# Optimization experiments

Measured on AMD Instinct MI355X. Metric: run time of the kernel, lower is better.

The kernel has to match this reference:

```python
import jax, jax.numpy as jnp
import numpy as np

EPS = 1e-8  # torch.cosine_similarity default eps


def setup_inputs() -> dict:
    key = jax.random.key(0)
    k1, k2 = jax.random.split(key)
    B, S, C, W = 8, 75, 64, 19
    support_x = jax.random.normal(k1, (B, S, C, W, W), dtype=jnp.float32)
    query_x = jax.random.normal(k2, (B, S, C, W, W), dtype=jnp.float32)
    return {"support_x": support_x, "query_x": query_x}


def reference(support_x, query_x):
    # support_x, query_x: [B, S, C, W, W]
    # For each support spatial location (i,j), cosine-similarity of its C-vector
    # against every query spatial location (p,q), then max over (p,q).
    B, S, C, W, _ = support_x.shape
    s_norm = jnp.linalg.norm(support_x, axis=2)  # [B,S,W,W]
    q_norm = jnp.linalg.norm(query_x, axis=2)    # [B,S,W,W]
    # Pairwise dot products over channels: [B,S,Wi,Wj,Wp,Wq]
    num = jnp.einsum('bscij,bscpq->bsijpq', support_x, query_x)
    denom = jnp.maximum(s_norm[:, :, :, :, None, None] * q_norm[:, :, None, None, :, :], EPS)
    sim = num / denom
    out = jnp.max(sim, axis=(-2, -1))  # max over query spatial grid -> [B,S,W,W]
    # loop order was i (rows) then j (cols), concatenated on last dim == row-major reshape
    return out.reshape(B, S, W * W)
```

## Files before the change

### kernel.cpp

```cpp
#include <hip/hip_runtime.h>
#include <hip/hip_bf16.h>
#include <stdint.h>

#define WW   361
#define CCH  64
#define MH   128
#define NP   368
#define NBS  600

typedef __attribute__((ext_vector_type(8))) short short8;
typedef __attribute__((ext_vector_type(4))) float f32x4;


__device__ __forceinline__ float stage_row(const float* __restrict__ gp,
                                           unsigned short* __restrict__ dst, int sw) {
  float a0 = 0.f, a1 = 0.f, a2 = 0.f, a3 = 0.f;
  #pragma unroll
  for (int h = 0; h < 2; ++h) {
    float v[32];
    #pragma unroll
    for (int j = 0; j < 32; ++j) v[j] = gp[(h * 32 + j) * WW];
    #pragma unroll
    for (int j = 0; j < 32; j += 4) {
      a0 += v[j] * v[j];     a1 += v[j+1] * v[j+1];
      a2 += v[j+2] * v[j+2]; a3 += v[j+3] * v[j+3];
    }
    #pragma unroll
    for (int c0 = 0; c0 < 4; ++c0) {
      const int c = h * 4 + c0;
      unsigned int u[4];
      #pragma unroll
      for (int jj = 0; jj < 4; ++jj) {
        __hip_bfloat162 b2 =
            __float22bfloat162_rn(make_float2(v[c0 * 8 + 2 * jj], v[c0 * 8 + 2 * jj + 1]));
        u[jj] = *(unsigned int*)&b2;
      }
      *(uint4*)&dst[(c ^ sw) * 8] = make_uint4(u[0], u[1], u[2], u[3]);
    }
  }
  return rsqrtf(a0 + a1 + a2 + a3);
}

__device__ __forceinline__ void zero_row(unsigned short* __restrict__ dst) {
  #pragma unroll
  for (int c = 0; c < 8; ++c)
    *(uint4*)&dst[c * 8] = make_uint4(0u, 0u, 0u, 0u);
}

__global__ __launch_bounds__(512, 4) void cossim_max_kernel(
    const float* __restrict__ support, const float* __restrict__ query,
    float* __restrict__ out)
{
  __shared__ __align__(16) unsigned short S_sh[MH * CCH];
  __shared__ __align__(16) unsigned short Q_sh[NP * CCH];
  __shared__ float inv_s[MH];
  __shared__ float inv_q[NP];

  const int tid   = threadIdx.x;
  const int bs    = blockIdx.x / 3;
  const int third = blockIdx.x % 3;
  const int mBase = third * MH;

  const float* sg = support + (size_t)bs * (WW * CCH);
  const float* qg = query   + (size_t)bs * (WW * CCH);

  if (tid < NP) {
    const int m = tid;
    if (m < WW) {
      inv_q[m] = stage_row(qg + m, &Q_sh[m * CCH], m & 7);
    } else {
      zero_row(&Q_sh[m * CCH]);
      inv_q[m] = 0.f;
    }
  } else if (tid < NP + MH) {
    const int mL = tid - NP;
    const int mG = mBase + mL;
    if (mG < WW) {
      inv_s[mL] = stage_row(sg + mG, &S_sh[mL * CCH], mL & 7);
    } else {
      zero_row(&S_sh[mL * CCH]);
      inv_s[mL] = 0.f;
    }
  }
  __syncthreads();

  const int lane = tid & 63;
  const int wv   = tid >> 6;
  const int l15  = lane & 15;
  const int quad = lane >> 4;

  short8 af[2];
  {
    const int m = 16 * wv + l15;
    #pragma unroll
    for (int s = 0; s < 2; ++s) {
      const int c = 4 * s + quad;
      af[s] = *(const short8*)&S_sh[m * CCH + ((c ^ (m & 7)) * 8)];
    }
  }

  f32x4 mx = {-3e38f, -3e38f, -3e38f, -3e38f};

  for (int pt = 0; pt < NP / 16; ++pt) {
    const int n  = 16 * pt + l15;
    const int sw = l15 & 7;
    short8 b0 = *(const short8*)&Q_sh[n * CCH + (((0 + quad) ^ sw) * 8)];
    short8 b1 = *(const short8*)&Q_sh[n * CCH + (((4 + quad) ^ sw) * 8)];
    f32x4 acc = {0.f, 0.f, 0.f, 0.f};
    acc = __builtin_amdgcn_mfma_f32_16x16x32_bf16(af[0], b0, acc, 0, 0, 0);
    acc = __builtin_amdgcn_mfma_f32_16x16x32_bf16(af[1], b1, acc, 0, 0, 0);
    const float qs   = inv_q[n];
    const float bias = (n < WW) ? 0.f : -1e30f;
    #pragma unroll
    for (int r = 0; r < 4; ++r) mx[r] = fmaxf(mx[r], acc[r] * qs + bias);
  }

  #pragma unroll
  for (int d = 1; d < 16; d <<= 1) {
    #pragma unroll
    for (int r = 0; r < 4; ++r) mx[r] = fmaxf(mx[r], __shfl_xor(mx[r], d));
  }

  if (l15 == 0) {
    #pragma unroll
    for (int r = 0; r < 4; ++r) {
      const int mL = 16 * wv + 4 * quad + r;
      const int iG = mBase + mL;
      if (iG < WW) out[(size_t)bs * WW + iG] = mx[r] * inv_s[mL];
    }
  }
}

extern "C" void kernel_launch(void* const* d_in, const int* in_sizes, int n_in,
                              void* d_out, int out_size, void* d_ws, size_t ws_size,
                              hipStream_t stream) {
  const float* support = (const float*)d_in[0];
  const float* query   = (const float*)d_in[1];
  float* out = (float*)d_out;
  dim3 grid(NBS * 3), block(512);
  hipLaunchKernelGGL(cossim_max_kernel, grid, block, 0, stream,
                     support, query, out);
}
```

Before: 140.9 us.

## Split each batch-slice into two 192-row blocks of 768 threads instead of three

Each (b,s) slice is now covered by two blocks of 192 support rows each, with 768 threads per block, where before it used three blocks of 128 rows. This cuts how often the query tile is staged and converted to bf16 in shared memory: 2 times per slice instead of 3, which removes a third of the redundant query loads. The staging routine is restructured to load and convert one 8-channel chunk at a time, keeping fewer values live in registers. The trade-off is larger blocks and a tighter register budget per thread from launch_bounds(768, 6).

```diff
diff --git a/kernel.cpp b/kernel.cpp
--- a/kernel.cpp
+++ b/kernel.cpp
@@ -4,9 +4,10 @@
 
 #define WW   361
 #define CCH  64
-#define MH   128
+#define MH   192
 #define NP   368
 #define NBS  600
+#define NTHR 768
 
 typedef __attribute__((ext_vector_type(8))) short short8;
 typedef __attribute__((ext_vector_type(4))) float f32x4;
@@ -16,29 +17,22 @@
                                            unsigned short* __restrict__ dst, int sw) {
   float a0 = 0.f, a1 = 0.f, a2 = 0.f, a3 = 0.f;
   #pragma unroll
-  for (int h = 0; h < 2; ++h) {
-    float v[32];
+  for (int c = 0; c < 8; ++c) {
+    float v[8];
     #pragma unroll
-    for (int j = 0; j < 32; ++j) v[j] = gp[(h * 32 + j) * WW];
+    for (int j = 0; j < 8; ++j) v[j] = gp[(c * 8 + j) * WW];
+    unsigned int u[4];
     #pragma unroll
-    for (int j = 0; j < 32; j += 4) {
-      a0 += v[j] * v[j];     a1 += v[j+1] * v[j+1];
-      a2 += v[j+2] * v[j+2]; a3 += v[j+3] * v[j+3];
+    for (int jj = 0; jj < 4; ++jj) {
+      a0 += v[2*jj] * v[2*jj];
+      a1 += v[2*jj+1] * v[2*jj+1];
+      __hip_bfloat162 b2 =
+          __float22bfloat162_rn(make_float2(v[2*jj], v[2*jj+1]));
+      u[jj] = *(unsigned int*)&b2;
     }
-    #pragma unroll
-    for (int c0 = 0; c0 < 4; ++c0) {
-      const int c = h * 4 + c0;
-      unsigned int u[4];
-      #pragma unroll
-      for (int jj = 0; jj < 4; ++jj) {
-        __hip_bfloat162 b2 =
-            __float22bfloat162_rn(make_float2(v[c0 * 8 + 2 * jj], v[c0 * 8 + 2 * jj + 1]));
-        u[jj] = *(unsigned int*)&b2;
-      }
-      *(uint4*)&dst[(c ^ sw) * 8] = make_uint4(u[0], u[1], u[2], u[3]);
-    }
+    *(uint4*)&dst[(c ^ sw) * 8] = make_uint4(u[0], u[1], u[2], u[3]);
   }
-  return rsqrtf(a0 + a1 + a2 + a3);
+  return rsqrtf((a0 + a1) + (a2 + a3));
 }
 
 __device__ __forceinline__ void zero_row(unsigned short* __restrict__ dst) {
@@ -47,7 +41,7 @@
     *(uint4*)&dst[c * 8] = make_uint4(0u, 0u, 0u, 0u);
 }
 
-__global__ __launch_bounds__(512, 4) void cossim_max_kernel(
+__global__ __launch_bounds__(NTHR, 6) void cossim_max_kernel(
     const float* __restrict__ support, const float* __restrict__ query,
     float* __restrict__ out)
 {
@@ -57,9 +51,9 @@
   __shared__ float inv_q[NP];
 
   const int tid   = threadIdx.x;
-  const int bs    = blockIdx.x / 3;
-  const int third = blockIdx.x % 3;
-  const int mBase = third * MH;
+  const int bs    = blockIdx.x >> 1;
+  const int half  = blockIdx.x & 1;
+  const int mBase = half * MH;
 
   const float* sg = support + (size_t)bs * (WW * CCH);
   const float* qg = query   + (size_t)bs * (WW * CCH);
@@ -137,7 +131,7 @@
   const float* support = (const float*)d_in[0];
   const float* query   = (const float*)d_in[1];
   float* out = (float*)d_out;
-  dim3 grid(NBS * 3), block(512);
+  dim3 grid(NBS * 2), block(NTHR);
   hipLaunchKernelGGL(cossim_max_kernel, grid, block, 0, stream,
                      support, query, out);
 }
```

Result: faster. 137.2 us (-2.6%).
